# Performance work log

Measured on AMD Instinct MI355X. Metric: run time of the kernel, lower is better.

Reference implementation:

```python
import jax, jax.numpy as jnp
import numpy as np

B, IN, OUT = 512, 4096, 11008


def setup_inputs() -> dict:
    key = jax.random.key(0)
    k_x, k_stored, k_sign, k_scale, k_bias = jax.random.split(key, 5)
    x = jax.random.normal(k_x, (B, IN), dtype=jnp.float32)
    # QINS encoding: stored uint8 magnitude in [1, 255], sign in {-1, +1}
    stored = jax.random.randint(k_stored, (OUT, IN), 1, 256, dtype=jnp.int32)
    sign = 2 * jax.random.randint(k_sign, (OUT, IN), 0, 2, dtype=jnp.int32) - 1
    # log-range from from_linear's fallback calibration: weights in [e^-10, e^0]
    log_min = jnp.asarray(-10.0, dtype=jnp.float32)
    log_max = jnp.asarray(0.0, dtype=jnp.float32)
    # per-channel calibration scale, clamped to [0.5, 2.0] in from_linear
    scale = jax.random.uniform(k_scale, (OUT,), dtype=jnp.float32, minval=0.5, maxval=2.0)
    bias = jax.random.normal(k_bias, (OUT,), dtype=jnp.float32) * 0.01
    return {"x": x, "stored": stored, "sign": sign, "log_min": log_min,
            "log_max": log_max, "scale": scale, "bias": bias}


def reference(x, stored, sign, log_min, log_max, scale, bias):
    # Reconstruct fp32 weight from log-scale uint8 encoding (QINS)
    normalized = (255.0 - stored.astype(jnp.float32)) / 254.0      # [OUT, IN]
    log_w = log_min + normalized * (log_max - log_min)
    weight = sign.astype(jnp.float32) * jnp.exp(log_w)             # [OUT, IN]
    # y = (x @ W^T + b) * scale   (per-output-channel scale)
    out = jnp.einsum('bi,oi->bo', x, weight) + bias
    return out * scale
```

## Files before the change

### kernel.cpp

```cpp
#include <hip/hip_runtime.h>
#include <hip/hip_bf16.h>

#define B_DIM   512
#define IN_DIM  4096
#define OUT_DIM 11008

typedef __bf16 bf16x4  __attribute__((ext_vector_type(4)));
typedef __bf16 bf16x8  __attribute__((ext_vector_type(8)));
typedef float  floatx4 __attribute__((ext_vector_type(4)));
typedef int    intx4   __attribute__((ext_vector_type(4)));

__global__ __launch_bounds__(256) void conv_x_kernel(
    const float* __restrict__ x, __bf16* __restrict__ xb) {
  int idx = blockIdx.x * blockDim.x + threadIdx.x;
  float4 v = ((const float4*)x)[idx];
  bf16x4 o;
  o[0] = (__bf16)v.x; o[1] = (__bf16)v.y; o[2] = (__bf16)v.z; o[3] = (__bf16)v.w;
  ((bf16x4*)xb)[idx] = o;
}

__global__ __launch_bounds__(512, 2) void fused_gemm_kernel(
    const __bf16* __restrict__ A,
    const int* __restrict__ stored,
    const int* __restrict__ sign,
    const float* __restrict__ logmin, const float* __restrict__ logmax,
    const float* __restrict__ scale, const float* __restrict__ bias,
    float* __restrict__ out) {
  constexpr int K = IN_DIM, N = OUT_DIM;
  constexpr int BK = 32;

  __shared__ __align__(16) __bf16 sB[2][64 * BK];

  const int tid  = threadIdx.x;
  const int lane = tid & 63;
  const int wave = tid >> 6;
  const int m16  = lane & 15;
  const int q    = lane >> 4;

  const int bn0 = blockIdx.x * 64;

  const float lmin  = logmin[0];
  const float slope = (logmax[0] - lmin) * (1.0f / 254.0f);

  const int br = tid >> 3;
  const int bc = (tid & 7) * 4;
  const int* gS = stored + (size_t)(bn0 + br) * K + bc;
  const int* gG = sign   + (size_t)(bn0 + br) * K + bc;

  const __bf16* gA = A + (size_t)(wave * 64 + m16) * K + q * 8;

  floatx4 acc[4][4] = {};

#define DECODE_STORE(sv, gv, dst)                                              \
  {                                                                            \
    bf16x4 wv;                                                                 \
    wv[0] = (__bf16)(__expf(fmaf((float)(255 - (sv).x), slope, lmin)) *        \
                     (float)(gv).x);                                           \
    wv[1] = (__bf16)(__expf(fmaf((float)(255 - (sv).y), slope, lmin)) *        \
                     (float)(gv).y);                                           \
    wv[2] = (__bf16)(__expf(fmaf((float)(255 - (sv).z), slope, lmin)) *        \
                     (float)(gv).z);                                           \
    wv[3] = (__bf16)(__expf(fmaf((float)(255 - (sv).w), slope, lmin)) *        \
                     (float)(gv).w);                                           \
    *(bf16x4*)(dst) = wv;                                                      \
  }

  intx4 sv = __builtin_nontemporal_load((const intx4*)(gS));
  intx4 gv = __builtin_nontemporal_load((const intx4*)(gG));
  bf16x8 afrA[4];
#pragma unroll
  for (int i = 0; i < 4; ++i)
    afrA[i] = *(const bf16x8*)(gA + (size_t)(i * 16) * K);
  DECODE_STORE(sv, gv, &sB[0][tid * 4]);
  intx4 s0 = __builtin_nontemporal_load((const intx4*)(gS + BK));
  intx4 g0 = __builtin_nontemporal_load((const intx4*)(gG + BK));
  intx4 s1 = __builtin_nontemporal_load((const intx4*)(gS + 2 * BK));
  intx4 g1 = __builtin_nontemporal_load((const intx4*)(gG + 2 * BK));

  int p = 0;
  for (int kt = 0; kt < K; kt += BK, p ^= 1) {
    __syncthreads();

    const bool more = (kt + BK) < K;

    bf16x8 afrB[4];
    if (more) {
#pragma unroll
      for (int i = 0; i < 4; ++i)
        afrB[i] = *(const bf16x8*)(gA + (size_t)(i * 16) * K + kt + BK);
    }

    bf16x8 bfr[4];
#pragma unroll
    for (int i = 0; i < 4; ++i)
      bfr[i] = *(const bf16x8*)&sB[p][(i * 16 + m16) * BK + q * 8];

    if (more) {
      DECODE_STORE(s0, g0, &sB[p ^ 1][tid * 4]);
      s0 = s1; g0 = g1;
      const int kt3 = (kt + 3 * BK) < K ? (kt + 3 * BK) : 0;
      s1 = __builtin_nontemporal_load((const intx4*)(gS + kt3));
      g1 = __builtin_nontemporal_load((const intx4*)(gG + kt3));
    }

#pragma unroll
    for (int mi = 0; mi < 4; ++mi)
#pragma unroll
      for (int ni = 0; ni < 4; ++ni)
        acc[mi][ni] = __builtin_amdgcn_mfma_f32_16x16x32_bf16(
            afrA[mi], bfr[ni], acc[mi][ni], 0, 0, 0);

    if (more) {
#pragma unroll
      for (int i = 0; i < 4; ++i) afrA[i] = afrB[i];
    }
  }

#pragma unroll
  for (int ni = 0; ni < 4; ++ni) {
    const int col = bn0 + ni * 16 + m16;
    const float sc = scale[col];
    const float bb = bias[col] * sc;
#pragma unroll
    for (int mi = 0; mi < 4; ++mi) {
#pragma unroll
      for (int r = 0; r < 4; ++r) {
        const int row = wave * 64 + mi * 16 + q * 4 + r;
        out[(size_t)row * N + col] = acc[mi][ni][r] * sc + bb;
      }
    }
  }
#undef DECODE_STORE
}

extern "C" void kernel_launch(void* const* d_in, const int* in_sizes, int n_in,
                              void* d_out, int out_size, void* d_ws, size_t ws_size,
                              hipStream_t stream) {
  const float* x      = (const float*)d_in[0];
  const int*   stored = (const int*)d_in[1];
  const int*   sign   = (const int*)d_in[2];
  const float* logmin = (const float*)d_in[3];
  const float* logmax = (const float*)d_in[4];
  const float* scale  = (const float*)d_in[5];
  const float* bias   = (const float*)d_in[6];
  float* out = (float*)d_out;

  __bf16* wsX = (__bf16*)d_ws;

  conv_x_kernel<<<(B_DIM * (IN_DIM / 4)) / 256, 256, 0, stream>>>(x, wsX);
  fused_gemm_kernel<<<OUT_DIM / 64, 512, 0, stream>>>(
      wsX, stored, sign, logmin, logmax, scale, bias, out);
}
```

Baseline: 530.7 us.

## Stage activations in shared memory and narrow output tile to 32 columns

The GEMM block now covers 32 output columns with 256 threads, four waves of 128 rows each. The activation tile is staged through double-buffered shared memory instead of each wave loading its A fragments straight from global memory into registers. The grid doubles to 344 blocks, which is meant to fill more CUs and make the weight decode per block cheaper. In exchange, every block re-reads the whole 512-row activation matrix, so L2 traffic for A doubles, and LDS use grows to about 64KB per block, which can limit occupancy.

```diff
diff --git a/kernel.cpp b/kernel.cpp
--- a/kernel.cpp
+++ b/kernel.cpp
@@ -19,7 +19,7 @@
   ((bf16x4*)xb)[idx] = o;
 }
 
-__global__ __launch_bounds__(512, 2) void fused_gemm_kernel(
+__global__ __launch_bounds__(256, 2) void fused_gemm_kernel(
     const __bf16* __restrict__ A,
     const int* __restrict__ stored,
     const int* __restrict__ sign,
@@ -29,7 +29,8 @@
   constexpr int K = IN_DIM, N = OUT_DIM;
   constexpr int BK = 32;
 
-  __shared__ __align__(16) __bf16 sB[2][64 * BK];
+  __shared__ __align__(16) __bf16 sA[2][512 * BK];
+  __shared__ __align__(16) __bf16 sB[2][32 * BK];
 
   const int tid  = threadIdx.x;
   const int lane = tid & 63;
@@ -37,19 +38,23 @@
   const int m16  = lane & 15;
   const int q    = lane >> 4;
 
-  const int bn0 = blockIdx.x * 64;
+  const int bn0 = blockIdx.x * 32;
 
   const float lmin  = logmin[0];
   const float slope = (logmax[0] - lmin) * (1.0f / 254.0f);
+
+  const int ar = tid >> 2;
+  const int ac = (tid & 3) * 8;
+  const __bf16* gA = A + (size_t)ar * K + ac;
+  const int lA = ar * BK + ac;
 
   const int br = tid >> 3;
   const int bc = (tid & 7) * 4;
   const int* gS = stored + (size_t)(bn0 + br) * K + bc;
   const int* gG = sign   + (size_t)(bn0 + br) * K + bc;
+  const int lB = br * BK + bc;
 
-  const __bf16* gA = A + (size_t)(wave * 64 + m16) * K + q * 8;
-
-  floatx4 acc[4][4] = {};
+  floatx4 acc[8][2] = {};
 
 #define DECODE_STORE(sv, gv, dst)                                              \
   {                                                                            \
@@ -65,13 +70,16 @@
     *(bf16x4*)(dst) = wv;                                                      \
   }
 
-  intx4 sv = __builtin_nontemporal_load((const intx4*)(gS));
-  intx4 gv = __builtin_nontemporal_load((const intx4*)(gG));
-  bf16x8 afrA[4];
+  {
+    intx4 sv = __builtin_nontemporal_load((const intx4*)gS);
+    intx4 gv = __builtin_nontemporal_load((const intx4*)gG);
 #pragma unroll
-  for (int i = 0; i < 4; ++i)
-    afrA[i] = *(const bf16x8*)(gA + (size_t)(i * 16) * K);
-  DECODE_STORE(sv, gv, &sB[0][tid * 4]);
+    for (int j = 0; j < 8; ++j) {
+      bf16x8 av = *(const bf16x8*)(gA + (size_t)(j * 64) * K);
+      *(bf16x8*)&sA[0][lA + j * 64 * BK] = av;
+    }
+    DECODE_STORE(sv, gv, &sB[0][lB]);
+  }
   intx4 s0 = __builtin_nontemporal_load((const intx4*)(gS + BK));
   intx4 g0 = __builtin_nontemporal_load((const intx4*)(gG + BK));
   intx4 s1 = __builtin_nontemporal_load((const intx4*)(gS + 2 * BK));
@@ -81,51 +89,49 @@
   for (int kt = 0; kt < K; kt += BK, p ^= 1) {
     __syncthreads();
 
-    const bool more = (kt + BK) < K;
+    const int ktA = (kt + BK) < K ? (kt + BK) : 0;
+    const int ktI = (kt + 3 * BK) < K ? (kt + 3 * BK) : 0;
 
-    bf16x8 afrB[4];
-    if (more) {
+    bf16x8 av[8];
 #pragma unroll
-      for (int i = 0; i < 4; ++i)
-        afrB[i] = *(const bf16x8*)(gA + (size_t)(i * 16) * K + kt + BK);
-    }
+    for (int j = 0; j < 8; ++j)
+      av[j] = *(const bf16x8*)(gA + (size_t)(j * 64) * K + ktA);
 
-    bf16x8 bfr[4];
+    bf16x8 afr[8], bfr[2];
 #pragma unroll
-    for (int i = 0; i < 4; ++i)
+    for (int i = 0; i < 8; ++i)
+      afr[i] = *(const bf16x8*)&sA[p][(wave * 128 + i * 16 + m16) * BK + q * 8];
+#pragma unroll
+    for (int i = 0; i < 2; ++i)
       bfr[i] = *(const bf16x8*)&sB[p][(i * 16 + m16) * BK + q * 8];
 
-    if (more) {
-      DECODE_STORE(s0, g0, &sB[p ^ 1][tid * 4]);
-      s0 = s1; g0 = g1;
-      const int kt3 = (kt + 3 * BK) < K ? (kt + 3 * BK) : 0;
-      s1 = __builtin_nontemporal_load((const intx4*)(gS + kt3));
-      g1 = __builtin_nontemporal_load((const intx4*)(gG + kt3));
-    }
+    DECODE_STORE(s0, g0, &sB[p ^ 1][lB]);
+    s0 = s1; g0 = g1;
+    s1 = __builtin_nontemporal_load((const intx4*)(gS + ktI));
+    g1 = __builtin_nontemporal_load((const intx4*)(gG + ktI));
 
 #pragma unroll
-    for (int mi = 0; mi < 4; ++mi)
+    for (int mi = 0; mi < 8; ++mi)
 #pragma unroll
-      for (int ni = 0; ni < 4; ++ni)
+      for (int ni = 0; ni < 2; ++ni)
         acc[mi][ni] = __builtin_amdgcn_mfma_f32_16x16x32_bf16(
-            afrA[mi], bfr[ni], acc[mi][ni], 0, 0, 0);
+            afr[mi], bfr[ni], acc[mi][ni], 0, 0, 0);
 
-    if (more) {
 #pragma unroll
-      for (int i = 0; i < 4; ++i) afrA[i] = afrB[i];
-    }
+    for (int j = 0; j < 8; ++j)
+      *(bf16x8*)&sA[p ^ 1][lA + j * 64 * BK] = av[j];
   }
 
 #pragma unroll
-  for (int ni = 0; ni < 4; ++ni) {
+  for (int ni = 0; ni < 2; ++ni) {
     const int col = bn0 + ni * 16 + m16;
     const float sc = scale[col];
     const float bb = bias[col] * sc;
 #pragma unroll
-    for (int mi = 0; mi < 4; ++mi) {
+    for (int mi = 0; mi < 8; ++mi) {
 #pragma unroll
       for (int r = 0; r < 4; ++r) {
-        const int row = wave * 64 + mi * 16 + q * 4 + r;
+        const int row = wave * 128 + mi * 16 + q * 4 + r;
         out[(size_t)row * N + col] = acc[mi][ni][r] * sc + bb;
       }
     }
@@ -148,6 +154,6 @@
   __bf16* wsX = (__bf16*)d_ws;
 
   conv_x_kernel<<<(B_DIM * (IN_DIM / 4)) / 256, 256, 0, stream>>>(x, wsX);
-  fused_gemm_kernel<<<OUT_DIM / 64, 512, 0, stream>>>(
+  fused_gemm_kernel<<<OUT_DIM / 32, 256, 0, stream>>>(
       wsX, stored, sign, logmin, logmax, scale, bias, out);
 }
```

Result: faster. 510.8 us (-3.7%).
